# Kernel tuning notes

Hardware: AMD Instinct MI355X
Metric: run time of the kernel (lower is better)

Reference implementation:

```python
import jax, jax.numpy as jnp
import numpy as np

DILATION_RATE = 4
SEGMENT_SIZE = 512


def setup_inputs() -> dict:
    key = jax.random.key(0)
    x = jax.random.normal(key, (4, 8192, 1024), dtype=jnp.float32)
    return {"x": x}


def reference(x):
    """LongNet-style dilated attention.

    For each offset in range(dilation_rate): take the strided slice
    x[:, offset::r, :], split it into segments of length `segment_size`,
    run full softmax(q k^T / sqrt(d)) v attention inside each segment
    (q=k=v=the slice; attention dim is the full d_model, matching how the
    original feeds [B, n_seg, seg, d_model] to FlashAttention), scatter the
    result back to the strided positions, and average the dilation heads
    (softmax over uniform logits == 1/r weights).

    Since seq_len % (r * segment_size) == 0, the r strided slices tile the
    sequence exactly, so we vectorize over offsets with a single reshape:
    position p = i*r + offset  ->  xr[:, i, offset, :].
    """
    r, seg = DILATION_RATE, SEGMENT_SIZE
    B, S, D = x.shape
    n = S // r            # tokens per strided slice
    g = n // seg          # segments per slice
    scale = 1.0 / jnp.sqrt(jnp.asarray(D, dtype=x.dtype))

    xs = x.reshape(B, g, seg, r, D)  # [B, g, seg, r, D]; axis r = dilation offset
    # segment-local attention, independently per (batch, offset, segment)
    scores = jnp.einsum("bgqrd,bgkrd->brgqk", xs, xs) * scale  # [B, r, g, seg, seg]
    probs = jax.nn.softmax(scores, axis=-1)
    out = jnp.einsum("brgqk,bgkrd->bgqrd", probs, xs)          # [B, g, seg, r, D]
    # scatter back to strided positions (pure reshape, since slices tile S),
    # then weighted sum with uniform softmax weights == divide by r.
    return out.reshape(B, S, D) / r
```

## Files before the change

kernel.cpp:

```cpp
#include <hip/hip_runtime.h>
#include <stdint.h>

typedef __bf16 bf16x8  __attribute__((ext_vector_type(8)));
typedef float  f32x4   __attribute__((ext_vector_type(4)));

#define LOG2E    1.44269504088896340736f
#define SM_SCALE 0.03125f

typedef __attribute__((address_space(1))) const uint32_t gau32;
typedef __attribute__((address_space(3))) uint32_t       lau32;
#define GLD16(g, l) __builtin_amdgcn_global_load_lds((gau32*)(g), (lau32*)(l), 16, 0, 0)

__device__ __forceinline__ uint32_t f2bf(float f) {
  uint32_t u = __builtin_bit_cast(uint32_t, f);
  u += 0x7FFFu + ((u >> 16) & 1u);
  return u >> 16;
}
__device__ __forceinline__ uint32_t pk2(float a, float b) {
  return f2bf(a) | (f2bf(b) << 16);
}
__device__ __forceinline__ uint4 pack8(float4 a, float4 b) {
  uint4 r;
  r.x = pk2(a.x, a.y); r.y = pk2(a.z, a.w);
  r.z = pk2(b.x, b.y); r.w = pk2(b.z, b.w);
  return r;
}

__global__ __launch_bounds__(256)
void prep_comb(const float* __restrict__ x, uint16_t* __restrict__ vt,
               uint16_t* __restrict__ xf) {
  __shared__ char tl[64 * 144];
  const int t    = threadIdx.x;
  const int blk  = blockIdx.x;
  const int dc   = blk & 15;
  const int kb   = (blk >> 4) & 7;
  const int prob = blk >> 7;
  const int b  = prob >> 4, off = (prob >> 2) & 3, gs = prob & 3;

  const int key = t >> 2, dq = t & 3;
  const float* src = x + ((size_t)(b * 8192 + gs * 2048 + (kb * 64 + key) * 4 + off)) * 1024
                     + dc * 64 + dq * 16;
  float4 f0 = *(const float4*)(src);
  float4 f1 = *(const float4*)(src + 4);
  float4 f2 = *(const float4*)(src + 8);
  float4 f3 = *(const float4*)(src + 12);
  const int swz = (key & 7) << 4;
  *(uint4*)(tl + key * 144 + ((dq * 32) ^ swz))      = pack8(f0, f1);
  *(uint4*)(tl + key * 144 + ((dq * 32 + 16) ^ swz)) = pack8(f2, f3);
  __syncthreads();
  {
    const int d = t >> 2, kq = t & 3;
    uint32_t w[8];
#pragma unroll
    for (int i = 0; i < 8; ++i) {
      int k0 = kq * 16 + 2 * i, k1 = k0 + 1;
      uint32_t a  = *(const uint16_t*)(tl + k0 * 144 + ((2 * d) ^ ((k0 & 7) << 4)));
      uint32_t bb = *(const uint16_t*)(tl + k1 * 144 + ((2 * d) ^ ((k1 & 7) << 4)));
      w[i] = a | (bb << 16);
    }
    uint16_t* dst = vt + ((size_t)(prob * 1024 + dc * 64 + d)) * 512 + kb * 64 + kq * 16;
    *(uint4*)(dst)     = *(uint4*)&w[0];
    *(uint4*)(dst + 8) = *(uint4*)&w[4];
  }
  {
    const int row = t >> 2, p = t & 3;
    const int dcl = p >> 1;
    const int dq8b = (p & 1) * 2;
    const int swz2 = (row & 7) << 4;
    char* fbase = (char*)xf +
        (((size_t)(prob * 32 + kb * 4 + (row >> 4)) * 32) + (dc * 2 + dcl)) * 1024;
#pragma unroll
    for (int i = 0; i < 2; ++i) {
      const int dq8 = dq8b + i;
      uint4 w = *(const uint4*)(tl + row * 144 + ((dcl * 64 + dq8 * 16) ^ swz2));
      *(uint4*)(fbase + ((row & 15) + 16 * dq8) * 16) = w;
    }
  }
}

#define RB_0 131072
#define RB_1 139264
#define LDSB_BYTES 147456

__global__ __launch_bounds__(1024, 4)
void dilattn11(const char* __restrict__ xf, const char* __restrict__ vt,
               float* __restrict__ out) {
  extern __shared__ char smem[];

  const int tid  = threadIdx.x;
  const int lane = tid & 63;
  const int wid  = tid >> 6;
  const int h    = lane >> 4;
  const int l15  = lane & 15;
  const int lane16 = lane * 16;

  const int blk  = blockIdx.x;
  const int jj   = blk >> 3;
  const int prob = ((blk & 7) << 3) + (jj >> 2);
  const int q0   = (jj & 3) * 128;
  const int b    = prob >> 4;
  const int off  = (prob >> 2) & 3;
  const int gs   = prob & 3;

  const char* xfp = xf + (size_t)prob * 1048576;
  const int qtile0 = q0 >> 4;
  const char* xfA = xfp + (size_t)(2 * wid) * 32768 + lane16;

  f32x4 S[2][8];
#pragma unroll
  for (int i = 0; i < 2; ++i)
#pragma unroll
    for (int j = 0; j < 8; ++j) S[i][j] = (f32x4){0.f, 0.f, 0.f, 0.f};

#pragma unroll 1
  for (int half = 0; half < 2; ++half) {
#pragma unroll
    for (int i = 0; i < 8; ++i) {
      const int c_ = wid * 8 + i;
      const int dcl = c_ >> 3, qt = c_ & 7;
      GLD16(xfp + ((size_t)(qtile0 + qt) * 32 + (half * 16 + dcl)) * 1024 + lane16,
            smem + dcl * 8192 + qt * 1024);
    }
    __syncthreads();
#pragma unroll
    for (int dc = 0; dc < 16; ++dc) {
      const int dca = half * 16 + dc;
      bf16x8 a0 = *(const bf16x8*)(xfA + dca * 1024);
      bf16x8 a1 = *(const bf16x8*)(xfA + 32768 + dca * 1024);
      const char* qb = smem + dc * 8192 + lane16;
      bf16x8 bq[8];
#pragma unroll
      for (int qt = 0; qt < 8; ++qt)
        bq[qt] = *(const bf16x8*)(qb + qt * 1024);
      __builtin_amdgcn_s_setprio(1);
#pragma unroll
      for (int qt = 0; qt < 8; ++qt) {
        S[0][qt] = __builtin_amdgcn_mfma_f32_16x16x32_bf16(a0, bq[qt], S[0][qt], 0, 0, 0);
        S[1][qt] = __builtin_amdgcn_mfma_f32_16x16x32_bf16(a1, bq[qt], S[1][qt], 0, 0, 0);
      }
      __builtin_amdgcn_s_setprio(0);
    }
    __syncthreads();
  }

  float mq[8], sq[8], rinv[8];
#pragma unroll
  for (int qt = 0; qt < 8; ++qt) {
    float m = S[0][qt][0];
#pragma unroll
    for (int kt = 0; kt < 2; ++kt)
#pragma unroll
      for (int r = 0; r < 4; ++r) m = fmaxf(m, S[kt][qt][r]);
    m = fmaxf(m, __shfl_xor(m, 16, 64));
    m = fmaxf(m, __shfl_xor(m, 32, 64));
    mq[qt] = m;
  }
  if (h == 0) {
#pragma unroll
    for (int qt = 0; qt < 8; ++qt)
      *(float*)(smem + RB_0 + (wid * 128 + qt * 16 + l15) * 4) = mq[qt];
  }
  __syncthreads();
#pragma unroll
  for (int qt = 0; qt < 8; ++qt) {
    float m = -3e38f;
#pragma unroll
    for (int w = 0; w < 16; ++w)
      m = fmaxf(m, *(const float*)(smem + RB_0 + (w * 128 + qt * 16 + l15) * 4));
    mq[qt] = m * SM_SCALE;
    sq[qt] = 0.f;
  }
#pragma unroll
  for (int kt = 0; kt < 2; ++kt)
#pragma unroll
    for (int qt = 0; qt < 8; ++qt)
#pragma unroll
      for (int r = 0; r < 4; ++r) {
        float v = exp2f((S[kt][qt][r] * SM_SCALE - mq[qt]) * LOG2E);
        S[kt][qt][r] = v;
        sq[qt] += v;
      }
#pragma unroll
  for (int qt = 0; qt < 8; ++qt) {
    sq[qt] += __shfl_xor(sq[qt], 16, 64);
    sq[qt] += __shfl_xor(sq[qt], 32, 64);
  }
  if (h == 0) {
#pragma unroll
    for (int qt = 0; qt < 8; ++qt)
      *(float*)(smem + RB_1 + (wid * 128 + qt * 16 + l15) * 4) = sq[qt];
  }
  __syncthreads();
#pragma unroll
  for (int qt = 0; qt < 8; ++qt) {
    float l = 0.f;
#pragma unroll
    for (int w = 0; w < 16; ++w)
      l += *(const float*)(smem + RB_1 + (w * 128 + qt * 16 + l15) * 4);
    rinv[qt] = 0.25f / l;
  }
#pragma unroll
  for (int kt = 0; kt < 2; ++kt)
#pragma unroll
    for (int qt = 0; qt < 8; ++qt) {
      uint2 w2;
      w2.x = pk2(S[kt][qt][0] * rinv[qt], S[kt][qt][1] * rinv[qt]);
      w2.y = pk2(S[kt][qt][2] * rinv[qt], S[kt][qt][3] * rinv[qt]);
      *(uint2*)(smem + qt * 16384 + wid * 1024 +
                (l15 + 16 * (2 * kt + (h >> 1))) * 16 + 8 * (h & 1)) = w2;
    }
  __syncthreads();

#pragma unroll 1
  for (int p = 0; p < 2; ++p) {
    const int dbase = p * 512 + 32 * wid;
    f32x4 acc[2][8];
#pragma unroll
    for (int i = 0; i < 2; ++i)
#pragma unroll
      for (int j = 0; j < 8; ++j) acc[i][j] = (f32x4){0.f, 0.f, 0.f, 0.f};

    const char* vtW = vt + (size_t)prob * 1048576 + (size_t)(dbase + l15) * 1024 + 16 * h;
#pragma unroll 1
    for (int ks = 0; ks < 16; ++ks) {
      bf16x8 v0 = *(const bf16x8*)(vtW + ks * 64);
      bf16x8 v1 = *(const bf16x8*)(vtW + 16384 + ks * 64);
      __builtin_amdgcn_s_setprio(1);
#pragma unroll
      for (int qp = 0; qp < 4; ++qp) {
        bf16x8 pa0 = *(const bf16x8*)(smem + (2 * qp) * 16384 + ks * 1024 + lane16);
        bf16x8 pa1 = *(const bf16x8*)(smem + (2 * qp + 1) * 16384 + ks * 1024 + lane16);
        acc[0][2 * qp]     = __builtin_amdgcn_mfma_f32_16x16x32_bf16(pa0, v0, acc[0][2 * qp], 0, 0, 0);
        acc[1][2 * qp]     = __builtin_amdgcn_mfma_f32_16x16x32_bf16(pa0, v1, acc[1][2 * qp], 0, 0, 0);
        acc[0][2 * qp + 1] = __builtin_amdgcn_mfma_f32_16x16x32_bf16(pa1, v0, acc[0][2 * qp + 1], 0, 0, 0);
        acc[1][2 * qp + 1] = __builtin_amdgcn_mfma_f32_16x16x32_bf16(pa1, v1, acc[1][2 * qp + 1], 0, 0, 0);
      }
      __builtin_amdgcn_s_setprio(0);
    }
    float* outW = out + ((size_t)(b * 8192 + gs * 2048 + (q0 + 4 * h) * 4 + off)) * 1024
                  + dbase + l15;
#pragma unroll
    for (int cd = 0; cd < 2; ++cd)
#pragma unroll
      for (int qt = 0; qt < 8; ++qt)
#pragma unroll
        for (int r = 0; r < 4; ++r)
          outW[(size_t)((16 * qt + r) * 4) * 1024 + cd * 16] = acc[cd][qt][r];
  }
}

#define KP_OFF 0
#define Q_OFF  65536
#define RED0   65536
#define RED1   67584
#define LDS_BYTES 73728

__global__ __launch_bounds__(256)
void vt_prepass(const float* __restrict__ x, uint16_t* __restrict__ vt) {
  __shared__ char tl[64 * 144];
  const int t    = threadIdx.x;
  const int blk  = blockIdx.x;
  const int dc   = blk & 15;
  const int kb   = (blk >> 4) & 7;
  const int prob = blk >> 7;
  const int b  = prob >> 4, off = (prob >> 2) & 3, gs = prob & 3;

  const int key = t >> 2, dq = t & 3;
  const float* src = x + ((size_t)(b * 8192 + gs * 2048 + (kb * 64 + key) * 4 + off)) * 1024
                     + dc * 64 + dq * 16;
  float4 f0 = *(const float4*)(src);
  float4 f1 = *(const float4*)(src + 4);
  float4 f2 = *(const float4*)(src + 8);
  float4 f3 = *(const float4*)(src + 12);
  const int swz = (key & 7) << 4;
  *(uint4*)(tl + key * 144 + ((dq * 32) ^ swz))      = pack8(f0, f1);
  *(uint4*)(tl + key * 144 + ((dq * 32 + 16) ^ swz)) = pack8(f2, f3);
  __syncthreads();
  const int d = t >> 2, kq = t & 3;
  uint32_t w[8];
#pragma unroll
  for (int i = 0; i < 8; ++i) {
    int k0 = kq * 16 + 2 * i, k1 = k0 + 1;
    uint32_t a  = *(const uint16_t*)(tl + k0 * 144 + ((2 * d) ^ ((k0 & 7) << 4)));
    uint32_t bb = *(const uint16_t*)(tl + k1 * 144 + ((2 * d) ^ ((k1 & 7) << 4)));
    w[i] = a | (bb << 16);
  }
  uint16_t* dst = vt + ((size_t)(prob * 1024 + dc * 64 + d)) * 512 + kb * 64 + kq * 16;
  *(uint4*)(dst)     = *(uint4*)&w[0];
  *(uint4*)(dst + 8) = *(uint4*)&w[4];
}

template <int USE_VT>
__global__ __launch_bounds__(512, 2)
void dilattn2(const float* __restrict__ x, const uint16_t* __restrict__ vt,
              float* __restrict__ out) {
  extern __shared__ char smem[];

  const int tid  = threadIdx.x;
  const int lane = tid & 63;
  const int wid  = tid >> 6;
  const int h    = lane >> 4;
  const int l15  = lane & 15;
  const int psw  = (l15 & 7) << 4;

  const int blk  = blockIdx.x;
  const int prob = blk >> 3;
  const int q0   = (blk & 7) * 64;
  const int b    = prob >> 4;
  const int off  = (prob >> 2) & 3;
  const int gs   = prob & 3;

  const float* xb = x + (size_t)b * (8192u * 1024u);

  const int srow = tid >> 3;
  const int sg   = tid & 7;
  const float* gK = xb + (size_t)(gs * 2048 + srow * 4 + off) * 1024 + sg * 8;
  const float* gQ = xb + (size_t)(gs * 2048 + (q0 + srow) * 4 + off) * 1024 + sg * 8;
  const int kWr = srow * 128 + ((sg * 16) ^ ((srow & 7) << 4));
  const int qWr = Q_OFF + kWr;

  const int akR = (64 * wid + l15) * 128;
  const int bqR = Q_OFF + l15 * 128;
  const int fb0 = (16 * h) ^ psw;

  f32x4 S[4][4];
#pragma unroll
  for (int i = 0; i < 4; ++i)
#pragma unroll
    for (int j = 0; j < 4; ++j) S[i][j] = (f32x4){0.f, 0.f, 0.f, 0.f};

  float4 kp[16], qp[2];
#pragma unroll
  for (int j = 0; j < 8; ++j) {
    const float* p = gK + (size_t)j * 262144;
    kp[2 * j]     = *(const float4*)(p);
    kp[2 * j + 1] = *(const float4*)(p + 4);
  }
  qp[0] = *(const float4*)(gQ);
  qp[1] = *(const float4*)(gQ + 4);

#pragma unroll 1
  for (int dc = 0; dc < 16; ++dc) {
#pragma unroll
    for (int j = 0; j < 8; ++j)
      *(uint4*)(smem + KP_OFF + kWr + j * 8192) = pack8(kp[2 * j], kp[2 * j + 1]);
    *(uint4*)(smem + qWr) = pack8(qp[0], qp[1]);
    if (dc < 15) {
      const int doff = (dc + 1) * 64;
#pragma unroll
      for (int j = 0; j < 8; ++j) {
        const float* p = gK + (size_t)j * 262144 + doff;
        kp[2 * j]     = *(const float4*)(p);
        kp[2 * j + 1] = *(const float4*)(p + 4);
      }
      qp[0] = *(const float4*)(gQ + doff);
      qp[1] = *(const float4*)(gQ + doff + 4);
    }
    __syncthreads();
#pragma unroll
    for (int s = 0; s < 2; ++s) {
      const int fb = fb0 ^ (s << 6);
      bf16x8 aK[4], bq[4];
#pragma unroll
      for (int kt = 0; kt < 4; ++kt)
        aK[kt] = *(const bf16x8*)(smem + akR + kt * 2048 + fb);
#pragma unroll
      for (int qt = 0; qt < 4; ++qt)
        bq[qt] = *(const bf16x8*)(smem + bqR + qt * 2048 + fb);
#pragma unroll
      for (int kt = 0; kt < 4; ++kt)
#pragma unroll
        for (int qt = 0; qt < 4; ++qt)
          S[kt][qt] = __builtin_amdgcn_mfma_f32_16x16x32_bf16(aK[kt], bq[qt], S[kt][qt], 0, 0, 0);
    }
    __syncthreads();
  }

  float mq[4], sq[4], rinv[4];
#pragma unroll
  for (int qt = 0; qt < 4; ++qt) {
    float m = S[0][qt][0];
#pragma unroll
    for (int kt = 0; kt < 4; ++kt)
#pragma unroll
      for (int r = 0; r < 4; ++r) m = fmaxf(m, S[kt][qt][r]);
    m = fmaxf(m, __shfl_xor(m, 16, 64));
    m = fmaxf(m, __shfl_xor(m, 32, 64));
    mq[qt] = m;
  }
  if (h == 0) {
#pragma unroll
    for (int qt = 0; qt < 4; ++qt)
      *(float*)(smem + RED0 + (wid * 64 + 16 * qt + l15) * 4) = mq[qt];
  }
  __syncthreads();
#pragma unroll
  for (int qt = 0; qt < 4; ++qt) {
    float m = -3e38f;
#pragma unroll
    for (int w = 0; w < 8; ++w)
      m = fmaxf(m, *(const float*)(smem + RED0 + (w * 64 + 16 * qt + l15) * 4));
    mq[qt] = m * SM_SCALE;
    sq[qt] = 0.f;
  }
#pragma unroll
  for (int kt = 0; kt < 4; ++kt)
#pragma unroll
    for (int qt = 0; qt < 4; ++qt)
#pragma unroll
      for (int r = 0; r < 4; ++r) {
        float v = exp2f((S[kt][qt][r] * SM_SCALE - mq[qt]) * LOG2E);
        S[kt][qt][r] = v;
        sq[qt] += v;
      }
#pragma unroll
  for (int qt = 0; qt < 4; ++qt) {
    sq[qt] += __shfl_xor(sq[qt], 16, 64);
    sq[qt] += __shfl_xor(sq[qt], 32, 64);
  }
  if (h == 0) {
#pragma unroll
    for (int qt = 0; qt < 4; ++qt)
      *(float*)(smem + RED1 + (wid * 64 + 16 * qt + l15) * 4) = sq[qt];
  }
  __syncthreads();
#pragma unroll
  for (int qt = 0; qt < 4; ++qt) {
    float l = 0.f;
#pragma unroll
    for (int w = 0; w < 8; ++w)
      l += *(const float*)(smem + RED1 + (w * 64 + 16 * qt + l15) * 4);
    rinv[qt] = 0.25f / l;
  }
#pragma unroll
  for (int kt = 0; kt < 4; ++kt)
#pragma unroll
    for (int qt = 0; qt < 4; ++qt) {
      uint2 w2;
      w2.x = pk2(S[kt][qt][0] * rinv[qt], S[kt][qt][1] * rinv[qt]);
      w2.y = pk2(S[kt][qt][2] * rinv[qt], S[kt][qt][3] * rinv[qt]);
      *(uint2*)(smem + KP_OFF + (16 * qt + l15) * 1024 +
                ((128 * wid + 32 * kt + 8 * h) ^ psw)) = w2;
    }
  __syncthreads();

  f32x4 acc[8][4];
#pragma unroll
  for (int i = 0; i < 8; ++i)
#pragma unroll
    for (int j = 0; j < 4; ++j) acc[i][j] = (f32x4){0.f, 0.f, 0.f, 0.f};

  const uint16_t* vtW = nullptr;
  if constexpr (USE_VT)
    vtW = vt + ((size_t)(prob * 1024 + 128 * wid + l15)) * 512 + 8 * h;

#pragma unroll 1
  for (int ks = 0; ks < 16; ++ks) {
    bf16x8 pa[4];
#pragma unroll
    for (int qt = 0; qt < 4; ++qt)
      pa[qt] = *(const bf16x8*)(smem + KP_OFF + (16 * qt + l15) * 1024 +
                                ((64 * ks + 16 * h) ^ psw));
#pragma unroll
    for (int cd = 0; cd < 8; ++cd) {
      bf16x8 v;
      if constexpr (USE_VT) {
        v = *(const bf16x8*)(vtW + (size_t)((cd >> 2) * 64 + (cd & 3) * 16) * 512 + 32 * ks);
      } else {
        const int d = 128 * wid + (cd >> 2) * 64 + (cd & 3) * 16 + l15;
        union { bf16x8 v; uint16_t u[8]; } a0;
#pragma unroll
        for (int jj = 0; jj < 8; ++jj) {
          int key = 32 * ks + 8 * h + jj;
          a0.u[jj] = (uint16_t)f2bf(xb[(size_t)(gs * 2048 + key * 4 + off) * 1024 + d]);
        }
        v = a0.v;
      }
#pragma unroll
      for (int qt = 0; qt < 4; ++qt)
        acc[cd][qt] = __builtin_amdgcn_mfma_f32_16x16x32_bf16(pa[qt], v, acc[cd][qt], 0, 0, 0);
    }
  }

#pragma unroll
  for (int cd = 0; cd < 8; ++cd) {
    const int d = 128 * wid + (cd >> 2) * 64 + (cd & 3) * 16 + l15;
#pragma unroll
    for (int qt = 0; qt < 4; ++qt)
#pragma unroll
      for (int r = 0; r < 4; ++r) {
        const int qq = q0 + 16 * qt + 4 * h + r;
        out[((size_t)(b * 8192 + gs * 2048 + qq * 4 + off)) * 1024 + d] = acc[cd][qt][r];
      }
  }
}

extern "C" void kernel_launch(void* const* d_in, const int* in_sizes, int n_in,
                              void* d_out, int out_size, void* d_ws, size_t ws_size,
                              hipStream_t stream) {
  const float* x = (const float*)d_in[0];
  float* out = (float*)d_out;
  (void)in_sizes; (void)n_in; (void)out_size;
  const size_t vt_bytes = 64ull * 1024 * 512 * 2;
  const size_t xf_bytes = 64ull * 1024 * 1024;
  if (ws_size >= vt_bytes + xf_bytes) {
    uint16_t* vtp = (uint16_t*)d_ws;
    uint16_t* xfp = (uint16_t*)((char*)d_ws + vt_bytes);
    hipFuncSetAttribute(reinterpret_cast<const void*>(dilattn11),
                        hipFuncAttributeMaxDynamicSharedMemorySize, LDSB_BYTES);
    prep_comb<<<8192, 256, 0, stream>>>(x, vtp, xfp);
    dilattn11<<<256, 1024, LDSB_BYTES, stream>>>((const char*)xfp, (const char*)vtp, out);
  } else if (ws_size >= vt_bytes) {
    uint16_t* vtp = (uint16_t*)d_ws;
    hipFuncSetAttribute(reinterpret_cast<const void*>(dilattn2<1>),
                        hipFuncAttributeMaxDynamicSharedMemorySize, LDS_BYTES);
    vt_prepass<<<8192, 256, 0, stream>>>(x, vtp);
    dilattn2<1><<<512, 512, LDS_BYTES, stream>>>(x, vtp, out);
  } else {
    hipFuncSetAttribute(reinterpret_cast<const void*>(dilattn2<0>),
                        hipFuncAttributeMaxDynamicSharedMemorySize, LDS_BYTES);
    dilattn2<0><<<512, 512, LDS_BYTES, stream>>>(x, nullptr, out);
  }
}
```

Baseline: 173.4 us.

## Halve attention block to 8 waves with 4 key tiles per wave

The main attention kernel now runs 512 threads (8 waves) per block instead of 1024. Each wave covers twice as many key rows in the QK^T phase and twice as many output columns in the PV phase. The cross-wave max and sum reductions shrink from 16 to 8 partials, and the P tile write indexing is remapped to match. The aim is more register-level reuse of each LDS-loaded Q/P fragment and fewer barrier participants. The cost is about twice the accumulator registers per wave and half as many waves available to hide latency.

```diff
diff --git a/kernel.cpp b/kernel.cpp
--- a/kernel.cpp
+++ b/kernel.cpp
@@ -78,12 +78,12 @@
   }
 }
 
-#define RB_0 131072
-#define RB_1 139264
-#define LDSB_BYTES 147456
-
-__global__ __launch_bounds__(1024, 4)
-void dilattn11(const char* __restrict__ xf, const char* __restrict__ vt,
+#define RC_0 131072
+#define RC_1 139264
+#define LDSC_BYTES 147456
+
+__global__ __launch_bounds__(512, 2)
+void dilattn12(const char* __restrict__ xf, const char* __restrict__ vt,
                float* __restrict__ out) {
   extern __shared__ char smem[];
 
@@ -104,19 +104,19 @@
 
   const char* xfp = xf + (size_t)prob * 1048576;
   const int qtile0 = q0 >> 4;
-  const char* xfA = xfp + (size_t)(2 * wid) * 32768 + lane16;
-
-  f32x4 S[2][8];
-#pragma unroll
-  for (int i = 0; i < 2; ++i)
+  const char* xfA = xfp + (size_t)(4 * wid) * 32768 + lane16;
+
+  f32x4 S[4][8];
+#pragma unroll
+  for (int i = 0; i < 4; ++i)
 #pragma unroll
     for (int j = 0; j < 8; ++j) S[i][j] = (f32x4){0.f, 0.f, 0.f, 0.f};
 
 #pragma unroll 1
   for (int half = 0; half < 2; ++half) {
 #pragma unroll
-    for (int i = 0; i < 8; ++i) {
-      const int c_ = wid * 8 + i;
+    for (int i = 0; i < 16; ++i) {
+      const int c_ = wid * 16 + i;
       const int dcl = c_ >> 3, qt = c_ & 7;
       GLD16(xfp + ((size_t)(qtile0 + qt) * 32 + (half * 16 + dcl)) * 1024 + lane16,
             smem + dcl * 8192 + qt * 1024);
@@ -127,6 +127,8 @@
       const int dca = half * 16 + dc;
       bf16x8 a0 = *(const bf16x8*)(xfA + dca * 1024);
       bf16x8 a1 = *(const bf16x8*)(xfA + 32768 + dca * 1024);
+      bf16x8 a2 = *(const bf16x8*)(xfA + 65536 + dca * 1024);
+      bf16x8 a3 = *(const bf16x8*)(xfA + 98304 + dca * 1024);
       const char* qb = smem + dc * 8192 + lane16;
       bf16x8 bq[8];
 #pragma unroll
@@ -137,6 +139,8 @@
       for (int qt = 0; qt < 8; ++qt) {
         S[0][qt] = __builtin_amdgcn_mfma_f32_16x16x32_bf16(a0, bq[qt], S[0][qt], 0, 0, 0);
         S[1][qt] = __builtin_amdgcn_mfma_f32_16x16x32_bf16(a1, bq[qt], S[1][qt], 0, 0, 0);
+        S[2][qt] = __builtin_amdgcn_mfma_f32_16x16x32_bf16(a2, bq[qt], S[2][qt], 0, 0, 0);
+        S[3][qt] = __builtin_amdgcn_mfma_f32_16x16x32_bf16(a3, bq[qt], S[3][qt], 0, 0, 0);
       }
       __builtin_amdgcn_s_setprio(0);
     }
@@ -148,7 +152,7 @@
   for (int qt = 0; qt < 8; ++qt) {
     float m = S[0][qt][0];
 #pragma unroll
-    for (int kt = 0; kt < 2; ++kt)
+    for (int kt = 0; kt < 4; ++kt)
 #pragma unroll
       for (int r = 0; r < 4; ++r) m = fmaxf(m, S[kt][qt][r]);
     m = fmaxf(m, __shfl_xor(m, 16, 64));
@@ -158,20 +162,20 @@
   if (h == 0) {
 #pragma unroll
     for (int qt = 0; qt < 8; ++qt)
-      *(float*)(smem + RB_0 + (wid * 128 + qt * 16 + l15) * 4) = mq[qt];
+      *(float*)(smem + RC_0 + (wid * 128 + qt * 16 + l15) * 4) = mq[qt];
   }
   __syncthreads();
 #pragma unroll
   for (int qt = 0; qt < 8; ++qt) {
     float m = -3e38f;
 #pragma unroll
-    for (int w = 0; w < 16; ++w)
-      m = fmaxf(m, *(const float*)(smem + RB_0 + (w * 128 + qt * 16 + l15) * 4));
+    for (int w = 0; w < 8; ++w)
+      m = fmaxf(m, *(const float*)(smem + RC_0 + (w * 128 + qt * 16 + l15) * 4));
     mq[qt] = m * SM_SCALE;
     sq[qt] = 0.f;
   }
 #pragma unroll
-  for (int kt = 0; kt < 2; ++kt)
+  for (int kt = 0; kt < 4; ++kt)
 #pragma unroll
     for (int qt = 0; qt < 8; ++qt)
 #pragma unroll
@@ -188,43 +192,45 @@
   if (h == 0) {
 #pragma unroll
     for (int qt = 0; qt < 8; ++qt)
-      *(float*)(smem + RB_1 + (wid * 128 + qt * 16 + l15) * 4) = sq[qt];
+      *(float*)(smem + RC_1 + (wid * 128 + qt * 16 + l15) * 4) = sq[qt];
   }
   __syncthreads();
 #pragma unroll
   for (int qt = 0; qt < 8; ++qt) {
     float l = 0.f;
 #pragma unroll
-    for (int w = 0; w < 16; ++w)
-      l += *(const float*)(smem + RB_1 + (w * 128 + qt * 16 + l15) * 4);
+    for (int w = 0; w < 8; ++w)
+      l += *(const float*)(smem + RC_1 + (w * 128 + qt * 16 + l15) * 4);
     rinv[qt] = 0.25f / l;
   }
 #pragma unroll
-  for (int kt = 0; kt < 2; ++kt)
+  for (int kt = 0; kt < 4; ++kt)
 #pragma unroll
     for (int qt = 0; qt < 8; ++qt) {
       uint2 w2;
       w2.x = pk2(S[kt][qt][0] * rinv[qt], S[kt][qt][1] * rinv[qt]);
       w2.y = pk2(S[kt][qt][2] * rinv[qt], S[kt][qt][3] * rinv[qt]);
-      *(uint2*)(smem + qt * 16384 + wid * 1024 +
-                (l15 + 16 * (2 * kt + (h >> 1))) * 16 + 8 * (h & 1)) = w2;
+      *(uint2*)(smem + qt * 16384 + (2 * wid + (kt >> 1)) * 1024 +
+                (l15 + 16 * (2 * (kt & 1) + (h >> 1))) * 16 + 8 * (h & 1)) = w2;
     }
   __syncthreads();
 
 #pragma unroll 1
   for (int p = 0; p < 2; ++p) {
-    const int dbase = p * 512 + 32 * wid;
-    f32x4 acc[2][8];
-#pragma unroll
-    for (int i = 0; i < 2; ++i)
+    const int dbase = p * 512 + 64 * wid;
+    f32x4 acc[4][8];
+#pragma unroll
+    for (int i = 0; i < 4; ++i)
 #pragma unroll
       for (int j = 0; j < 8; ++j) acc[i][j] = (f32x4){0.f, 0.f, 0.f, 0.f};
 
     const char* vtW = vt + (size_t)prob * 1048576 + (size_t)(dbase + l15) * 1024 + 16 * h;
 #pragma unroll 1
     for (int ks = 0; ks < 16; ++ks) {
-      bf16x8 v0 = *(const bf16x8*)(vtW + ks * 64);
-      bf16x8 v1 = *(const bf16x8*)(vtW + 16384 + ks * 64);
+      bf16x8 v0 = *(const bf16x8*)(vtW + 0 * 16384 + ks * 64);
+      bf16x8 v1 = *(const bf16x8*)(vtW + 1 * 16384 + ks * 64);
+      bf16x8 v2 = *(const bf16x8*)(vtW + 2 * 16384 + ks * 64);
+      bf16x8 v3 = *(const bf16x8*)(vtW + 3 * 16384 + ks * 64);
       __builtin_amdgcn_s_setprio(1);
 #pragma unroll
       for (int qp = 0; qp < 4; ++qp) {
@@ -232,15 +238,19 @@
         bf16x8 pa1 = *(const bf16x8*)(smem + (2 * qp + 1) * 16384 + ks * 1024 + lane16);
         acc[0][2 * qp]     = __builtin_amdgcn_mfma_f32_16x16x32_bf16(pa0, v0, acc[0][2 * qp], 0, 0, 0);
         acc[1][2 * qp]     = __builtin_amdgcn_mfma_f32_16x16x32_bf16(pa0, v1, acc[1][2 * qp], 0, 0, 0);
+        acc[2][2 * qp]     = __builtin_amdgcn_mfma_f32_16x16x32_bf16(pa0, v2, acc[2][2 * qp], 0, 0, 0);
+        acc[3][2 * qp]     = __builtin_amdgcn_mfma_f32_16x16x32_bf16(pa0, v3, acc[3][2 * qp], 0, 0, 0);
         acc[0][2 * qp + 1] = __builtin_amdgcn_mfma_f32_16x16x32_bf16(pa1, v0, acc[0][2 * qp + 1], 0, 0, 0);
         acc[1][2 * qp + 1] = __builtin_amdgcn_mfma_f32_16x16x32_bf16(pa1, v1, acc[1][2 * qp + 1], 0, 0, 0);
+        acc[2][2 * qp + 1] = __builtin_amdgcn_mfma_f32_16x16x32_bf16(pa1, v2, acc[2][2 * qp + 1], 0, 0, 0);
+        acc[3][2 * qp + 1] = __builtin_amdgcn_mfma_f32_16x16x32_bf16(pa1, v3, acc[3][2 * qp + 1], 0, 0, 0);
       }
       __builtin_amdgcn_s_setprio(0);
     }
     float* outW = out + ((size_t)(b * 8192 + gs * 2048 + (q0 + 4 * h) * 4 + off)) * 1024
                   + dbase + l15;
 #pragma unroll
-    for (int cd = 0; cd < 2; ++cd)
+    for (int cd = 0; cd < 4; ++cd)
 #pragma unroll
       for (int qt = 0; qt < 8; ++qt)
 #pragma unroll
@@ -506,10 +516,10 @@
   if (ws_size >= vt_bytes + xf_bytes) {
     uint16_t* vtp = (uint16_t*)d_ws;
     uint16_t* xfp = (uint16_t*)((char*)d_ws + vt_bytes);
-    hipFuncSetAttribute(reinterpret_cast<const void*>(dilattn11),
-                        hipFuncAttributeMaxDynamicSharedMemorySize, LDSB_BYTES);
+    hipFuncSetAttribute(reinterpret_cast<const void*>(dilattn12),
+                        hipFuncAttributeMaxDynamicSharedMemorySize, LDSC_BYTES);
     prep_comb<<<8192, 256, 0, stream>>>(x, vtp, xfp);
-    dilattn11<<<256, 1024, LDSB_BYTES, stream>>>((const char*)xfp, (const char*)vtp, out);
+    dilattn12<<<256, 512, LDSC_BYTES, stream>>>((const char*)xfp, (const char*)vtp, out);
   } else if (ws_size >= vt_bytes) {
     uint16_t* vtp = (uint16_t*)d_ws;
     hipFuncSetAttribute(reinterpret_cast<const void*>(dilattn2<1>),
```

After: 164.6 us (median of 2 runs). 1.05x faster.
